# Kernel optimization log

Hardware: AMD Instinct MI355X
Metric: run time of the kernel (lower is better)

Reference implementation:

```python
import jax, jax.numpy as jnp
import numpy as np

T, B, H, E, V = 128, 64, 512, 256, 32000
UNK = 2
EPS = 1e-10


def setup_inputs() -> dict:
    key = jax.random.key(0)
    ks = jax.random.split(key, 16)
    s = 0.02
    return {
        "u_enc_out": jax.random.normal(ks[0], (T, B, H), jnp.float32),
        "z_tm1": jax.random.randint(ks[1], (1, B), 0, V),
        "last_hidden": jax.random.normal(ks[2], (1, B, H), jnp.float32),
        "u_input": jax.random.randint(ks[3], (T, B), 0, V),
        "emb": jax.random.normal(ks[4], (V, E), jnp.float32) * s,
        "attn_W": jax.random.normal(ks[5], (H, 2 * H), jnp.float32) * s,
        "attn_b": jnp.zeros((H,), jnp.float32),
        "attn_v": jax.random.normal(ks[6], (H,), jnp.float32) * (1.0 / np.sqrt(H)),
        "gru_Wih": jax.random.normal(ks[7], (3 * H, H + E), jnp.float32) * s,
        "gru_Whh": jax.random.normal(ks[8], (3 * H, H), jnp.float32) * s,
        "gru_bih": jnp.zeros((3 * H,), jnp.float32),
        "gru_bhh": jnp.zeros((3 * H,), jnp.float32),
        "proj_W": jax.random.normal(ks[9], (V, 2 * H), jnp.float32) * s,
        "proj_b": jnp.zeros((V,), jnp.float32),
        "copy1_W": jax.random.normal(ks[10], (H, H), jnp.float32) * s,
        "copy1_b": jnp.zeros((H,), jnp.float32),
    }


def _copy_logscore(raw, u_input):
    # raw: [B,T] copy scores; u_input: [T,B] int ids
    # Faithful to: log(bmm(exp(raw - max), sparse_one_hot_with_1e-10_floor)) + max
    cmax = jnp.max(raw, axis=1, keepdims=True)            # [B,1]
    ex = jnp.exp(raw - cmax)                              # [B,T]
    idx = u_input.T                                       # [B,T]
    idx = jnp.where(idx == UNK, V + jnp.arange(T)[None, :], idx)
    mask = (u_input.T != 0).astype(ex.dtype)
    total = jnp.sum(ex, axis=1)                           # [B] (all t, incl. ignored)
    scat = jax.vmap(lambda e, i: jnp.zeros((V + T,), ex.dtype).at[i].add(e))(ex * mask, idx)
    return jnp.log(EPS * total[:, None] + (1.0 - EPS) * scat) + cmax  # [B,V+T]


def reference(u_enc_out, z_tm1, last_hidden, u_input, emb, attn_W, attn_b, attn_v,
              gru_Wih, gru_Whh, gru_bih, gru_bhh, proj_W, proj_b, copy1_W, copy1_b):
    enc = jnp.transpose(u_enc_out, (1, 0, 2))             # [B,T,H]
    h = last_hidden[0]                                    # [B,H]
    # Attn: energy = tanh(Linear([h;enc])), score = v . energy, softmax over T
    Hrep = jnp.broadcast_to(h[:, None, :], enc.shape)
    energy = jnp.tanh(jnp.einsum('bti,hi->bth', jnp.concatenate([Hrep, enc], -1), attn_W) + attn_b)
    alpha = jax.nn.softmax(jnp.einsum('h,bth->bt', attn_v, energy), axis=1)
    ctx = jnp.einsum('bt,bth->bh', alpha, enc)            # [B,H]
    # GRU step (pytorch gate order r,z,n)
    x = jnp.concatenate([emb[z_tm1[0]], ctx], axis=-1)    # [B,E+H]
    gi = x @ gru_Wih.T + gru_bih
    gh = h @ gru_Whh.T + gru_bhh
    i_r, i_z, i_n = jnp.split(gi, 3, axis=-1)
    h_r, h_z, h_n = jnp.split(gh, 3, axis=-1)
    r = jax.nn.sigmoid(i_r + h_r)
    z = jax.nn.sigmoid(i_z + h_z)
    n = jnp.tanh(i_n + r * h_n)
    h_new = (1.0 - z) * n + z * h                         # [B,H]
    gru_out = h_new[None]                                 # [1,B,H]
    new_hidden = h_new[None]
    # generation score
    gen_score = jnp.concatenate([h_new, ctx], -1) @ proj_W.T + proj_b  # [B,V]
    # copy score
    cs = jnp.tanh(jnp.einsum('bth,ih->bti', enc, copy1_W) + copy1_b)   # [B,T,H]
    raw = jnp.einsum('bth,bh->bt', cs, h_new)             # [B,T]
    u_copy = _copy_logscore(raw, u_input)                 # [B,V+T]
    scores = jax.nn.softmax(jnp.concatenate([gen_score, u_copy], axis=1), axis=1)
    g, c = scores[:, :V], scores[:, V:]                   # [B,V], [B,V+T]
    proba = jnp.concatenate([g + c[:, :V], c[:, V:]], axis=1)  # [B,V+T]
    return gru_out, new_hidden, proba
```

## Files before the change

kernel.cpp:

```cpp
#include <hip/hip_runtime.h>
#include <math.h>

#define T_ 128
#define B_ 64
#define H_ 512
#define E_ 256
#define V_ 32000
#define VT_ (V_ + T_)
#define UNK_ 2
#define EPS_ 1e-10f
#define NP_ (V_ / 64)

typedef __attribute__((ext_vector_type(8))) _Float16 half8;
typedef __attribute__((ext_vector_type(2))) _Float16 half2v;
typedef __attribute__((ext_vector_type(4))) float floatx4;

#define NB_ZERO 32
#define NB_CVTA 512
#define NB_CVTC 512
#define NB_WH   8192
#define NB_CVTW 2048
#define NB_XE   64
#define NB_XH   128
#define NB_BC   8
#define NB_PRO (NB_ZERO + NB_CVTA + NB_CVTC + NB_WH + NB_CVTW + NB_XE + NB_XH + NB_BC)

__global__ __launch_bounds__(256) void prologue_k(
        const float* __restrict__ attn_W,
        const float* __restrict__ copy1_W, const float* __restrict__ last_h,
        const float* __restrict__ attn_b, const float* __restrict__ emb,
        const int* __restrict__ z, const float* __restrict__ Wih,
        const float* __restrict__ Whh, const float* __restrict__ bih,
        const float* __restrict__ bhh,
        float* __restrict__ zbase,
        _Float16* __restrict__ Wb_attn, _Float16* __restrict__ Wb_copy,
        float* __restrict__ Wh, _Float16* __restrict__ Wcat,
        _Float16* __restrict__ xg, float* __restrict__ bcat) {
    int bid = blockIdx.x, tid = threadIdx.x;
    if (bid < NB_ZERO) { zbase[bid * 256 + tid] = 0.f; return; }
    bid -= NB_ZERO;
    if (bid < NB_CVTA) {
        int c = tid * 2;
        float2 v = *(const float2*)(attn_W + (size_t)bid * 1024 + 512 + c);
        Wb_attn[bid * 512 + c]     = (_Float16)v.x;
        Wb_attn[bid * 512 + c + 1] = (_Float16)v.y;
        return;
    }
    bid -= NB_CVTA;
    if (bid < NB_CVTC) {
        int c = tid * 2;
        float2 v = *(const float2*)(copy1_W + (size_t)bid * 512 + c);
        Wb_copy[bid * 512 + c]     = (_Float16)v.x;
        Wb_copy[bid * 512 + c + 1] = (_Float16)v.y;
        return;
    }
    bid -= NB_CVTC;
    if (bid < NB_WH) {
        int wid = bid * 4 + (tid >> 6), lane = tid & 63;
        int b = wid >> 9, m = wid & 511;
        const float4* wr = (const float4*)(attn_W + (size_t)m * 1024);
        const float4* xr = (const float4*)(last_h + b * 512);
        float s = 0.f;
        #pragma unroll
        for (int i = 0; i < 2; ++i) {
            int k = lane + i * 64;
            float4 w = wr[k], x = xr[k];
            s += w.x * x.x + w.y * x.y + w.z * x.z + w.w * x.w;
        }
        #pragma unroll
        for (int off = 32; off > 0; off >>= 1) s += __shfl_down(s, off);
        if (lane == 0) Wh[b * 512 + m] = s + attn_b[m];
        return;
    }
    bid -= NB_WH;
    if (bid < NB_CVTW) {
        int mp = bid;
        int q  = (mp >> 4) & 3;
        int hh = (mp >> 6) * 16 + (mp & 15);
        #pragma unroll
        for (int j = 0; j < 5; ++j) {
            int c = j * 256 + tid;
            float w;
            if (q == 0)      w = (c < 768) ? Wih[(size_t)hh * 768 + c]
                                           : Whh[(size_t)hh * 512 + (c - 768)];
            else if (q == 1) w = (c < 768) ? Wih[(size_t)(512 + hh) * 768 + c]
                                           : Whh[(size_t)(512 + hh) * 512 + (c - 768)];
            else if (q == 2) w = (c < 768) ? Wih[(size_t)(1024 + hh) * 768 + c] : 0.f;
            else             w = (c >= 768) ? Whh[(size_t)(1024 + hh) * 512 + (c - 768)] : 0.f;
            Wcat[(size_t)mp * 1280 + c] = (_Float16)w;
        }
        return;
    }
    bid -= NB_CVTW;
    if (bid < NB_XE) {
        int idx = bid * 256 + tid;
        int bb = idx >> 8, c = idx & 255;
        xg[bb * 1280 + c] = (_Float16)emb[(size_t)z[bb] * E_ + c];
        return;
    }
    bid -= NB_XE;
    if (bid < NB_XH) {
        int idx = bid * 256 + tid;
        int bb = idx >> 9, c = idx & 511;
        xg[bb * 1280 + 768 + c] = (_Float16)last_h[bb * H_ + c];
        return;
    }
    bid -= NB_XH;
    {
        int mp = bid * 256 + tid;
        int q  = (mp >> 4) & 3;
        int hh = (mp >> 6) * 16 + (mp & 15);
        float v2;
        if (q == 0)      v2 = bih[hh] + bhh[hh];
        else if (q == 1) v2 = bih[512 + hh] + bhh[512 + hh];
        else if (q == 2) v2 = bih[1024 + hh];
        else             v2 = bhh[1024 + hh];
        bcat[mp] = v2;
    }
}

__global__ __launch_bounds__(512) void enc_dual_k(
        const float* __restrict__ u_enc,
        const _Float16* __restrict__ Wa,
        const _Float16* __restrict__ Wc,
        const float* __restrict__ Wh,
        const float* __restrict__ attn_v,
        const float* __restrict__ copy1_b,
        float* __restrict__ score,
        _Float16* __restrict__ cs) {
    __shared__ _Float16 As[64 * 512];
    int bid = blockIdx.x;
    int xcd = bid & 7, loc = bid >> 3;
    int xt = xcd * 16 + (loc & 15);
    int yt = loc >> 4;
    int b  = xt >> 1;
    int t0 = (xt & 1) * 64;
    int r0 = b * T_ + t0;
    int tid = threadIdx.x;
    int lane = tid & 63, wave = tid >> 6;
    const float* srcb = u_enc + (size_t)t0 * B_ * H_ + (size_t)b * H_;
    #pragma unroll
    for (int i = 0; i < 8; ++i) {
        int G = i * 512 + tid;
        int r = G >> 6, s = G & 63;
        const float4* p = (const float4*)(srcb + (size_t)r * B_ * H_ + s * 8);
        float4 a0 = p[0], a1 = p[1];
        half8 v;
        v[0] = (_Float16)a0.x; v[1] = (_Float16)a0.y; v[2] = (_Float16)a0.z; v[3] = (_Float16)a0.w;
        v[4] = (_Float16)a1.x; v[5] = (_Float16)a1.y; v[6] = (_Float16)a1.z; v[7] = (_Float16)a1.w;
        *(half8*)&As[(size_t)(((r << 6) | (s ^ (r & 7))) << 3)] = v;
    }
    __syncthreads();
    int n0 = yt * 128 + (wave >> 2) * 64 + (wave & 3) * 16;
    int coln = lane & 15;
    int g = lane >> 4;
    const _Float16* wra = Wa + (size_t)(n0 + coln) * H_ + g * 8;
    const _Float16* wrc = Wc + (size_t)(n0 + coln) * H_ + g * 8;
    floatx4 acca[4] = {}, accc[4] = {};
    #pragma unroll 4
    for (int k0 = 0; k0 < H_; k0 += 32) {
        half8 fba = *(const half8*)(wra + k0);
        half8 fbc = *(const half8*)(wrc + k0);
        #pragma unroll
        for (int mi = 0; mi < 4; ++mi) {
            int r = mi * 16 + coln;
            half8 fa = *(const half8*)&As[((size_t)r << 9) +
                          ((((k0 >> 3) + g) ^ (coln & 7)) << 3)];
            acca[mi] = __builtin_amdgcn_mfma_f32_16x16x32_f16(fa, fba, acca[mi], 0, 0, 0);
            accc[mi] = __builtin_amdgcn_mfma_f32_16x16x32_f16(fa, fbc, accc[mi], 0, 0, 0);
        }
    }
    int col = n0 + coln;
    float addt = Wh[b * H_ + col];
    float av   = attn_v[col];
    float cb   = copy1_b[col];
    int rbase = g * 4;
    #pragma unroll
    for (int mi = 0; mi < 4; ++mi)
        #pragma unroll
        for (int r = 0; r < 4; ++r) {
            int row = r0 + mi * 16 + rbase + r;
            float x = acca[mi][r] + addt;
            float t2 = __expf(2.f * x);
            float v = av * ((t2 - 1.f) / (t2 + 1.f));
            v += __shfl_xor(v, 1);
            v += __shfl_xor(v, 2);
            v += __shfl_xor(v, 4);
            v += __shfl_xor(v, 8);
            if (coln == 0) atomicAdd(&score[row], v);
            float y = accc[mi][r] + cb;
            float t3 = __expf(2.f * y);
            cs[(size_t)row * H_ + col] = (_Float16)((t3 - 1.f) / (t3 + 1.f));
        }
}

__global__ __launch_bounds__(128) void softctx_k(
        const float* __restrict__ score, const float* __restrict__ u_enc,
        _Float16* __restrict__ xcat, _Float16* __restrict__ xg) {
    __shared__ float al[T_];
    __shared__ float red[T_];
    int b = blockIdx.x, tid = threadIdx.x;
    float v = score[b * T_ + tid];
    red[tid] = v;
    __syncthreads();
    for (int s = 64; s > 0; s >>= 1) { if (tid < s) red[tid] = fmaxf(red[tid], red[tid + s]); __syncthreads(); }
    float m = red[0]; __syncthreads();
    float e = __expf(v - m);
    red[tid] = e;
    __syncthreads();
    for (int s = 64; s > 0; s >>= 1) { if (tid < s) red[tid] += red[tid + s]; __syncthreads(); }
    al[tid] = e / red[0];
    __syncthreads();
    int col0 = blockIdx.y * 256 + tid * 2;
    const float2* ebase = (const float2*)(u_enc + (size_t)b * H_ + col0);
    float s0 = 0.f, s1 = 0.f;
    #pragma unroll 16
    for (int t = 0; t < T_; ++t) {
        float2 u = ebase[(size_t)t * (B_ * H_ / 2)];
        float a = al[t];
        s0 += a * u.x;
        s1 += a * u.y;
    }
    half2v o; o[0] = (_Float16)s0; o[1] = (_Float16)s1;
    *(half2v*)(xcat + b * 1024 + 512 + col0) = o;
    *(half2v*)(xg + b * 1280 + 256 + col0)   = o;
}

__global__ __launch_bounds__(512) void grucat_k(
        const _Float16* __restrict__ xg,
        const _Float16* __restrict__ Wcat,
        const float* __restrict__ bcat,
        const float* __restrict__ hprev,
        float* __restrict__ out,
        _Float16* __restrict__ xcat) {
    __shared__ float Lt[8][64][17];
    int tid = threadIdx.x;
    int lane = tid & 63, wave = tid >> 6;
    int q = wave & 3, khalf = wave >> 2;
    int n0 = blockIdx.x * 64 + q * 16;
    int coln = lane & 15;
    int kq  = (lane >> 4) * 8;
    int kbase = khalf * 640;
    const _Float16* wrow  = Wcat + (size_t)(n0 + coln) * 1280 + kbase + kq;
    const _Float16* abase = xg + kbase + kq;
    floatx4 acc[4] = {};
    #pragma unroll 5
    for (int k0 = 0; k0 < 640; k0 += 32) {
        half8 fb = *(const half8*)(wrow + k0);
        #pragma unroll
        for (int mi = 0; mi < 4; ++mi) {
            half8 fa = *(const half8*)(abase + (size_t)(mi * 16 + coln) * 1280 + k0);
            acc[mi] = __builtin_amdgcn_mfma_f32_16x16x32_f16(fa, fb, acc[mi], 0, 0, 0);
        }
    }
    int rbase = (lane >> 4) * 4;
    #pragma unroll
    for (int mi = 0; mi < 4; ++mi)
        #pragma unroll
        for (int r = 0; r < 4; ++r)
            Lt[wave][mi * 16 + rbase + r][coln] = acc[mi][r];
    __syncthreads();
    int HB = blockIdx.x * 16;
    #pragma unroll
    for (int p = tid; p < 1024; p += 512) {
        int b = p >> 4, i = p & 15;
        float G0 = Lt[0][b][i] + Lt[4][b][i] + bcat[blockIdx.x * 64 + i];
        float G1 = Lt[1][b][i] + Lt[5][b][i] + bcat[blockIdx.x * 64 + 16 + i];
        float G2 = Lt[2][b][i] + Lt[6][b][i] + bcat[blockIdx.x * 64 + 32 + i];
        float G3 = Lt[3][b][i] + Lt[7][b][i] + bcat[blockIdx.x * 64 + 48 + i];
        float rr = 1.f / (1.f + __expf(-G0));
        float zz = 1.f / (1.f + __expf(-G1));
        float nn = tanhf(G2 + rr * G3);
        float h  = hprev[b * H_ + HB + i];
        float hv = (1.f - zz) * nn + zz * h;
        out[b * H_ + HB + i] = hv;
        out[B_ * H_ + b * H_ + HB + i] = hv;
        xcat[b * 1024 + HB + i] = (_Float16)hv;
    }
}

__global__ __launch_bounds__(256) void proj_stats_k(
        const _Float16* __restrict__ xcat,
        const float* __restrict__ Wp,
        const float* __restrict__ bp,
        float* __restrict__ gen,
        float* __restrict__ mpart, float* __restrict__ lpart) {
    __shared__ float m_lds[4][64];
    __shared__ float l_lds[4][64];
    int lane = threadIdx.x & 63;
    int wave = threadIdx.x >> 6;
    int n0 = (blockIdx.x * 4 + wave) * 16;
    int coln = lane & 15;
    int kq  = (lane >> 4) * 8;
    const float* wrow = Wp + (size_t)(n0 + coln) * 1024 + kq;
    const _Float16* abase = xcat + kq;
    floatx4 acc[4] = {};
    #pragma unroll 8
    for (int k0 = 0; k0 < 1024; k0 += 32) {
        const float4* wb = (const float4*)(wrow + k0);
        float4 w0 = wb[0], w1 = wb[1];
        half8 fb;
        fb[0] = (_Float16)w0.x; fb[1] = (_Float16)w0.y; fb[2] = (_Float16)w0.z; fb[3] = (_Float16)w0.w;
        fb[4] = (_Float16)w1.x; fb[5] = (_Float16)w1.y; fb[6] = (_Float16)w1.z; fb[7] = (_Float16)w1.w;
        #pragma unroll
        for (int mi = 0; mi < 4; ++mi) {
            half8 fa = *(const half8*)(abase + (size_t)(mi * 16 + coln) * 1024 + k0);
            acc[mi] = __builtin_amdgcn_mfma_f32_16x16x32_f16(fa, fb, acc[mi], 0, 0, 0);
        }
    }
    int rbase = (lane >> 4) * 4;
    float bias = bp[n0 + coln];
    #pragma unroll
    for (int mi = 0; mi < 4; ++mi)
        #pragma unroll
        for (int r = 0; r < 4; ++r) {
            int brow = mi * 16 + rbase + r;
            float x = acc[mi][r] + bias;
            gen[(size_t)brow * V_ + n0 + coln] = x;
            float mm = x;
            mm = fmaxf(mm, __shfl_xor(mm, 1));
            mm = fmaxf(mm, __shfl_xor(mm, 2));
            mm = fmaxf(mm, __shfl_xor(mm, 4));
            mm = fmaxf(mm, __shfl_xor(mm, 8));
            float e = __expf(x - mm);
            e += __shfl_xor(e, 1);
            e += __shfl_xor(e, 2);
            e += __shfl_xor(e, 4);
            e += __shfl_xor(e, 8);
            if (coln == 0) { m_lds[wave][brow] = mm; l_lds[wave][brow] = e; }
        }
    __syncthreads();
    if (threadIdx.x < 64) {
        int bb = threadIdx.x;
        float M = m_lds[0][bb], L = l_lds[0][bb];
        #pragma unroll
        for (int w = 1; w < 4; ++w) {
            float m2 = m_lds[w][bb], l2 = l_lds[w][bb];
            float nm = fmaxf(M, m2);
            L = L * __expf(M - nm) + l2 * __expf(m2 - nm);
            M = nm;
        }
        mpart[bb * NP_ + blockIdx.x] = M;
        lpart[bb * NP_ + blockIdx.x] = L;
    }
}

__global__ __launch_bounds__(512) void raw_epi_k(
        const _Float16* __restrict__ cs, const float* __restrict__ hnew,
        const int* __restrict__ u_input,
        const float* __restrict__ mpart, const float* __restrict__ lpart,
        float* __restrict__ scat, float* __restrict__ params) {
    __shared__ float rawS[T_];
    __shared__ float red[T_];
    __shared__ float ms[512], ls[512];
    int b = blockIdx.x, tid = threadIdx.x;
    int lane = tid & 63, wave = tid >> 6;
    const float4* hp = (const float4*)(hnew + b * H_ + lane * 8);
    float4 ha = hp[0], hb = hp[1];
    #pragma unroll 4
    for (int i = 0; i < 16; ++i) {
        int t = wave * 16 + i;
        half8 c8 = *(const half8*)(cs + (size_t)(b * T_ + t) * H_ + lane * 8);
        float s = (float)c8[0] * ha.x + (float)c8[1] * ha.y + (float)c8[2] * ha.z + (float)c8[3] * ha.w
                + (float)c8[4] * hb.x + (float)c8[5] * hb.y + (float)c8[6] * hb.z + (float)c8[7] * hb.w;
        #pragma unroll
        for (int off = 32; off > 0; off >>= 1) s += __shfl_down(s, off);
        if (lane == 0) rawS[t] = s;
    }
    __syncthreads();
    int t = tid;
    float v = (t < T_) ? rawS[t] : -1e30f;
    if (t < T_) red[t] = v;
    __syncthreads();
    for (int s = 64; s > 0; s >>= 1) { if (t < s) red[t] = fmaxf(red[t], red[t + s]); __syncthreads(); }
    float cm = red[0]; __syncthreads();
    float e = (t < T_) ? __expf(v - cm) : 0.f;
    if (t < T_) red[t] = e;
    __syncthreads();
    for (int s = 64; s > 0; s >>= 1) { if (t < s) red[t] += red[t + s]; __syncthreads(); }
    float tot = red[0]; __syncthreads();
    int id = (t < T_) ? u_input[t * B_ + b] : 0;
    size_t j = (size_t)b * VT_ + ((id == UNK_) ? (V_ + t) : id);
    if (id != 0) scat[j] = 0.f;
    __syncthreads();
    if (id != 0) atomicAdd(&scat[j], e);
    if (t < T_) red[t] = (id != 0) ? e : 0.f;
    __syncthreads();
    for (int s = 64; s > 0; s >>= 1) { if (t < s) red[t] += red[t + s]; __syncthreads(); }
    float ssum = red[0]; __syncthreads();
    float sv = (id != 0) ? scat[j] : 0.f;
    if (t < T_) red[t] = sv;
    __syncthreads();
    for (int s = 64; s > 0; s >>= 1) { if (t < s) red[t] = fmaxf(red[t], red[t + s]); __syncthreads(); }
    float smax = red[0]; __syncthreads();
    float M = -1e30f, L = 0.f;
    if (t < NP_) { M = mpart[b * NP_ + t]; L = lpart[b * NP_ + t]; }
    ms[t] = M; ls[t] = L;
    __syncthreads();
    for (int s = 256; s > 0; s >>= 1) {
        if (t < s) {
            float m2 = ms[t + s], l2 = ls[t + s];
            float nm = fmaxf(ms[t], m2);
            ls[t] = ls[t] * __expf(ms[t] - nm) + l2 * __expf(m2 - nm);
            ms[t] = nm;
        }
        __syncthreads();
    }
    if (t == 0) {
        float Mg = ms[0], Zg = ls[0];
        float umax = cm + logf(EPS_ * tot + (1.f - EPS_) * smax);
        float M2 = fmaxf(Mg, umax);
        float coef = __expf(cm - M2);
        float Z = Zg * __expf(Mg - M2) + coef * (EPS_ * tot * (float)VT_ + (1.f - EPS_) * ssum);
        float invZ = 1.f / Z;
        params[b * 4 + 0] = M2;
        params[b * 4 + 1] = invZ;
        params[b * 4 + 2] = coef * EPS_ * tot * invZ;
        params[b * 4 + 3] = coef * (1.f - EPS_) * invZ;
    }
}

__global__ __launch_bounds__(256) void write_k(const float* __restrict__ gen,
                                               const float* __restrict__ params,
                                               float* __restrict__ proba) {
    int b = blockIdx.y;
    int i4 = blockIdx.x * 256 + threadIdx.x;
    if (i4 >= VT_ / 4) return;
    float M = params[b * 4], invZ = params[b * 4 + 1], addc = params[b * 4 + 2];
    int j = i4 * 4;
    float4 p;
    if (j < V_) {
        float4 g = *(const float4*)(gen + (size_t)b * V_ + j);
        p.x = addc + __expf(g.x - M) * invZ;
        p.y = addc + __expf(g.y - M) * invZ;
        p.z = addc + __expf(g.z - M) * invZ;
        p.w = addc + __expf(g.w - M) * invZ;
    } else {
        p.x = p.y = p.z = p.w = addc;
    }
    *(float4*)(proba + (size_t)b * VT_ + j) = p;
}

__global__ void fix_k(const float* __restrict__ gen, const float* __restrict__ scat,
                      const int* __restrict__ u_input, const float* __restrict__ params,
                      float* __restrict__ proba) {
    int b = blockIdx.x, t = threadIdx.x;
    int id = u_input[t * B_ + b];
    if (id == 0) return;
    int j = (id == UNK_) ? (V_ + t) : id;
    float M = params[b * 4], invZ = params[b * 4 + 1];
    float addc = params[b * 4 + 2], scoef = params[b * 4 + 3];
    float p = addc + scoef * scat[(size_t)b * VT_ + j];
    if (j < V_) p += __expf(gen[(size_t)b * V_ + j] - M) * invZ;
    proba[(size_t)b * VT_ + j] = p;
}

extern "C" void kernel_launch(void* const* d_in, const int* in_sizes, int n_in,
                              void* d_out, int out_size, void* d_ws, size_t ws_size,
                              hipStream_t stream) {
    const float* u_enc   = (const float*)d_in[0];
    const int*   z_tm1   = (const int*)d_in[1];
    const float* last_h  = (const float*)d_in[2];
    const int*   u_input = (const int*)d_in[3];
    const float* emb     = (const float*)d_in[4];
    const float* attn_W  = (const float*)d_in[5];
    const float* attn_b  = (const float*)d_in[6];
    const float* attn_v  = (const float*)d_in[7];
    const float* gru_Wih = (const float*)d_in[8];
    const float* gru_Whh = (const float*)d_in[9];
    const float* gru_bih = (const float*)d_in[10];
    const float* gru_bhh = (const float*)d_in[11];
    const float* proj_W  = (const float*)d_in[12];
    const float* proj_b  = (const float*)d_in[13];
    const float* copy1_W = (const float*)d_in[14];
    const float* copy1_b = (const float*)d_in[15];
    float* out = (float*)d_out;

    float* ws    = (float*)d_ws;
    float* score = ws;
    float* gen   = score + B_ * T_;
    float* scat  = gen + (size_t)B_ * V_;
    float* Wh    = scat + (size_t)B_ * VT_;
    float* mpart = Wh + B_ * H_;
    float* lpart = mpart + B_ * NP_;
    float* params= lpart + B_ * NP_;
    float* bcat  = params + B_ * 4;
    _Float16* xcat  = (_Float16*)(bcat + 2048);
    _Float16* xg    = xcat + B_ * 1024;
    _Float16* Wb_attn = xg + B_ * 1280;
    _Float16* Wb_copy = Wb_attn + H_ * H_;
    _Float16* Wcat  = Wb_copy + H_ * H_;
    _Float16* cs    = Wcat + 2048 * 1280;

    prologue_k<<<NB_PRO, 256, 0, stream>>>(attn_W, copy1_W, last_h, attn_b,
                                           emb, z_tm1, gru_Wih, gru_Whh, gru_bih, gru_bhh,
                                           score, Wb_attn, Wb_copy, Wh, Wcat, xg, bcat);

    enc_dual_k<<<512, 512, 0, stream>>>(u_enc, Wb_attn, Wb_copy, Wh, attn_v, copy1_b,
                                        score, cs);

    softctx_k<<<dim3(B_, 2), 128, 0, stream>>>(score, u_enc, xcat, xg);

    grucat_k<<<32, 512, 0, stream>>>(xg, Wcat, bcat, last_h, out, xcat);

    proj_stats_k<<<NP_, 256, 0, stream>>>(xcat, proj_W, proj_b, gen, mpart, lpart);

    raw_epi_k<<<B_, 512, 0, stream>>>(cs, out, u_input, mpart, lpart, scat, params);

    float* proba = out + 2 * B_ * H_;
    write_k<<<dim3((VT_ / 4 + 255) / 256, B_), 256, 0, stream>>>(gen, params, proba);
    fix_k<<<B_, T_, 0, stream>>>(gen, scat, u_input, params, proba);
}
```

Baseline: 355.5 us.

## Fuse copy-score epilogue into projection launch and merge write with fix

The copy-score raw/scatter blocks now run as extra blocks of the projection GEMM launch, so the two run concurrently instead of back to back. The final softmax normalisation is folded into a combined write+fix kernel. Each block of that kernel redundantly reduces the 500 partial max/sum pairs for its row, then writes probabilities and patches copied positions inside its own 1024-element range. This removes two kernel launches and their serialization. The cost is redundant per-block reductions and heterogeneous blocks within one grid.

Measured after the change: 353.5 us. Within noise of the previous version (-0.6%).

```diff
diff --git a/kernel.cpp b/kernel.cpp
--- a/kernel.cpp
+++ b/kernel.cpp
@@ -279,87 +279,87 @@
     }
 }
 
-__global__ __launch_bounds__(256) void proj_stats_k(
+__global__ __launch_bounds__(256) void proj_raw_k(
         const _Float16* __restrict__ xcat,
         const float* __restrict__ Wp,
         const float* __restrict__ bp,
         float* __restrict__ gen,
-        float* __restrict__ mpart, float* __restrict__ lpart) {
+        float* __restrict__ mpart, float* __restrict__ lpart,
+        const _Float16* __restrict__ cs,
+        const float* __restrict__ hnew,
+        const int* __restrict__ u_input,
+        float* __restrict__ scat, float* __restrict__ sc4) {
     __shared__ float m_lds[4][64];
     __shared__ float l_lds[4][64];
-    int lane = threadIdx.x & 63;
-    int wave = threadIdx.x >> 6;
-    int n0 = (blockIdx.x * 4 + wave) * 16;
-    int coln = lane & 15;
-    int kq  = (lane >> 4) * 8;
-    const float* wrow = Wp + (size_t)(n0 + coln) * 1024 + kq;
-    const _Float16* abase = xcat + kq;
-    floatx4 acc[4] = {};
-    #pragma unroll 8
-    for (int k0 = 0; k0 < 1024; k0 += 32) {
-        const float4* wb = (const float4*)(wrow + k0);
-        float4 w0 = wb[0], w1 = wb[1];
-        half8 fb;
-        fb[0] = (_Float16)w0.x; fb[1] = (_Float16)w0.y; fb[2] = (_Float16)w0.z; fb[3] = (_Float16)w0.w;
-        fb[4] = (_Float16)w1.x; fb[5] = (_Float16)w1.y; fb[6] = (_Float16)w1.z; fb[7] = (_Float16)w1.w;
-        #pragma unroll
-        for (int mi = 0; mi < 4; ++mi) {
-            half8 fa = *(const half8*)(abase + (size_t)(mi * 16 + coln) * 1024 + k0);
-            acc[mi] = __builtin_amdgcn_mfma_f32_16x16x32_f16(fa, fb, acc[mi], 0, 0, 0);
-        }
-    }
-    int rbase = (lane >> 4) * 4;
-    float bias = bp[n0 + coln];
-    #pragma unroll
-    for (int mi = 0; mi < 4; ++mi)
-        #pragma unroll
-        for (int r = 0; r < 4; ++r) {
-            int brow = mi * 16 + rbase + r;
-            float x = acc[mi][r] + bias;
-            gen[(size_t)brow * V_ + n0 + coln] = x;
-            float mm = x;
-            mm = fmaxf(mm, __shfl_xor(mm, 1));
-            mm = fmaxf(mm, __shfl_xor(mm, 2));
-            mm = fmaxf(mm, __shfl_xor(mm, 4));
-            mm = fmaxf(mm, __shfl_xor(mm, 8));
-            float e = __expf(x - mm);
-            e += __shfl_xor(e, 1);
-            e += __shfl_xor(e, 2);
-            e += __shfl_xor(e, 4);
-            e += __shfl_xor(e, 8);
-            if (coln == 0) { m_lds[wave][brow] = mm; l_lds[wave][brow] = e; }
-        }
-    __syncthreads();
-    if (threadIdx.x < 64) {
-        int bb = threadIdx.x;
-        float M = m_lds[0][bb], L = l_lds[0][bb];
-        #pragma unroll
-        for (int w = 1; w < 4; ++w) {
-            float m2 = m_lds[w][bb], l2 = l_lds[w][bb];
-            float nm = fmaxf(M, m2);
-            L = L * __expf(M - nm) + l2 * __expf(m2 - nm);
-            M = nm;
-        }
-        mpart[bb * NP_ + blockIdx.x] = M;
-        lpart[bb * NP_ + blockIdx.x] = L;
-    }
-}
-
-__global__ __launch_bounds__(512) void raw_epi_k(
-        const _Float16* __restrict__ cs, const float* __restrict__ hnew,
-        const int* __restrict__ u_input,
-        const float* __restrict__ mpart, const float* __restrict__ lpart,
-        float* __restrict__ scat, float* __restrict__ params) {
     __shared__ float rawS[T_];
     __shared__ float red[T_];
-    __shared__ float ms[512], ls[512];
-    int b = blockIdx.x, tid = threadIdx.x;
+    if (blockIdx.x < NP_) {
+        int lane = threadIdx.x & 63;
+        int wave = threadIdx.x >> 6;
+        int n0 = (blockIdx.x * 4 + wave) * 16;
+        int coln = lane & 15;
+        int kq  = (lane >> 4) * 8;
+        const float* wrow = Wp + (size_t)(n0 + coln) * 1024 + kq;
+        const _Float16* abase = xcat + kq;
+        floatx4 acc[4] = {};
+        #pragma unroll 8
+        for (int k0 = 0; k0 < 1024; k0 += 32) {
+            const float4* wb = (const float4*)(wrow + k0);
+            float4 w0 = wb[0], w1 = wb[1];
+            half8 fb;
+            fb[0] = (_Float16)w0.x; fb[1] = (_Float16)w0.y; fb[2] = (_Float16)w0.z; fb[3] = (_Float16)w0.w;
+            fb[4] = (_Float16)w1.x; fb[5] = (_Float16)w1.y; fb[6] = (_Float16)w1.z; fb[7] = (_Float16)w1.w;
+            #pragma unroll
+            for (int mi = 0; mi < 4; ++mi) {
+                half8 fa = *(const half8*)(abase + (size_t)(mi * 16 + coln) * 1024 + k0);
+                acc[mi] = __builtin_amdgcn_mfma_f32_16x16x32_f16(fa, fb, acc[mi], 0, 0, 0);
+            }
+        }
+        int rbase = (lane >> 4) * 4;
+        float bias = bp[n0 + coln];
+        #pragma unroll
+        for (int mi = 0; mi < 4; ++mi)
+            #pragma unroll
+            for (int r = 0; r < 4; ++r) {
+                int brow = mi * 16 + rbase + r;
+                float x = acc[mi][r] + bias;
+                gen[(size_t)brow * V_ + n0 + coln] = x;
+                float mm = x;
+                mm = fmaxf(mm, __shfl_xor(mm, 1));
+                mm = fmaxf(mm, __shfl_xor(mm, 2));
+                mm = fmaxf(mm, __shfl_xor(mm, 4));
+                mm = fmaxf(mm, __shfl_xor(mm, 8));
+                float e = __expf(x - mm);
+                e += __shfl_xor(e, 1);
+                e += __shfl_xor(e, 2);
+                e += __shfl_xor(e, 4);
+                e += __shfl_xor(e, 8);
+                if (coln == 0) { m_lds[wave][brow] = mm; l_lds[wave][brow] = e; }
+            }
+        __syncthreads();
+        if (threadIdx.x < 64) {
+            int bb = threadIdx.x;
+            float M = m_lds[0][bb], L = l_lds[0][bb];
+            #pragma unroll
+            for (int w = 1; w < 4; ++w) {
+                float m2 = m_lds[w][bb], l2 = l_lds[w][bb];
+                float nm = fmaxf(M, m2);
+                L = L * __expf(M - nm) + l2 * __expf(m2 - nm);
+                M = nm;
+            }
+            mpart[bb * NP_ + blockIdx.x] = M;
+            lpart[bb * NP_ + blockIdx.x] = L;
+        }
+        return;
+    }
+    int b = blockIdx.x - NP_;
+    int tid = threadIdx.x;
     int lane = tid & 63, wave = tid >> 6;
     const float4* hp = (const float4*)(hnew + b * H_ + lane * 8);
     float4 ha = hp[0], hb = hp[1];
     #pragma unroll 4
-    for (int i = 0; i < 16; ++i) {
-        int t = wave * 16 + i;
+    for (int i = 0; i < 32; ++i) {
+        int t = wave * 32 + i;
         half8 c8 = *(const half8*)(cs + (size_t)(b * T_ + t) * H_ + lane * 8);
         float s = (float)c8[0] * ha.x + (float)c8[1] * ha.y + (float)c8[2] * ha.z + (float)c8[3] * ha.w
                 + (float)c8[4] * hb.x + (float)c8[5] * hb.y + (float)c8[6] * hb.z + (float)c8[7] * hb.w;
@@ -392,67 +392,84 @@
     if (t < T_) red[t] = sv;
     __syncthreads();
     for (int s = 64; s > 0; s >>= 1) { if (t < s) red[t] = fmaxf(red[t], red[t + s]); __syncthreads(); }
-    float smax = red[0]; __syncthreads();
+    if (t == 0) {
+        sc4[b * 4 + 0] = cm;
+        sc4[b * 4 + 1] = tot;
+        sc4[b * 4 + 2] = ssum;
+        sc4[b * 4 + 3] = red[0];
+    }
+}
+
+__global__ __launch_bounds__(256) void write_fix_k(
+        const float* __restrict__ gen,
+        const float* __restrict__ mpart, const float* __restrict__ lpart,
+        const float* __restrict__ sc4, const int* __restrict__ u_input,
+        const float* __restrict__ scat, float* __restrict__ proba) {
+    __shared__ float ms[256], ls[256];
+    __shared__ float pb[4];
+    int b = blockIdx.y, tid = threadIdx.x;
     float M = -1e30f, L = 0.f;
-    if (t < NP_) { M = mpart[b * NP_ + t]; L = lpart[b * NP_ + t]; }
-    ms[t] = M; ls[t] = L;
-    __syncthreads();
-    for (int s = 256; s > 0; s >>= 1) {
-        if (t < s) {
-            float m2 = ms[t + s], l2 = ls[t + s];
-            float nm = fmaxf(ms[t], m2);
-            ls[t] = ls[t] * __expf(ms[t] - nm) + l2 * __expf(m2 - nm);
-            ms[t] = nm;
+    for (int s = tid; s < NP_; s += 256) {
+        float m2 = mpart[b * NP_ + s], l2 = lpart[b * NP_ + s];
+        float nm = fmaxf(M, m2);
+        L = L * __expf(M - nm) + l2 * __expf(m2 - nm);
+        M = nm;
+    }
+    ms[tid] = M; ls[tid] = L;
+    __syncthreads();
+    for (int s = 128; s > 0; s >>= 1) {
+        if (tid < s) {
+            float m2 = ms[tid + s], l2 = ls[tid + s];
+            float nm = fmaxf(ms[tid], m2);
+            ls[tid] = ls[tid] * __expf(ms[tid] - nm) + l2 * __expf(m2 - nm);
+            ms[tid] = nm;
         }
         __syncthreads();
     }
-    if (t == 0) {
+    if (tid == 0) {
         float Mg = ms[0], Zg = ls[0];
+        float cm = sc4[b * 4], tot = sc4[b * 4 + 1], ssum = sc4[b * 4 + 2], smax = sc4[b * 4 + 3];
         float umax = cm + logf(EPS_ * tot + (1.f - EPS_) * smax);
         float M2 = fmaxf(Mg, umax);
         float coef = __expf(cm - M2);
         float Z = Zg * __expf(Mg - M2) + coef * (EPS_ * tot * (float)VT_ + (1.f - EPS_) * ssum);
         float invZ = 1.f / Z;
-        params[b * 4 + 0] = M2;
-        params[b * 4 + 1] = invZ;
-        params[b * 4 + 2] = coef * EPS_ * tot * invZ;
-        params[b * 4 + 3] = coef * (1.f - EPS_) * invZ;
-    }
-}
-
-__global__ __launch_bounds__(256) void write_k(const float* __restrict__ gen,
-                                               const float* __restrict__ params,
-                                               float* __restrict__ proba) {
-    int b = blockIdx.y;
-    int i4 = blockIdx.x * 256 + threadIdx.x;
-    if (i4 >= VT_ / 4) return;
-    float M = params[b * 4], invZ = params[b * 4 + 1], addc = params[b * 4 + 2];
-    int j = i4 * 4;
-    float4 p;
-    if (j < V_) {
-        float4 g = *(const float4*)(gen + (size_t)b * V_ + j);
-        p.x = addc + __expf(g.x - M) * invZ;
-        p.y = addc + __expf(g.y - M) * invZ;
-        p.z = addc + __expf(g.z - M) * invZ;
-        p.w = addc + __expf(g.w - M) * invZ;
-    } else {
-        p.x = p.y = p.z = p.w = addc;
-    }
-    *(float4*)(proba + (size_t)b * VT_ + j) = p;
-}
-
-__global__ void fix_k(const float* __restrict__ gen, const float* __restrict__ scat,
-                      const int* __restrict__ u_input, const float* __restrict__ params,
-                      float* __restrict__ proba) {
-    int b = blockIdx.x, t = threadIdx.x;
-    int id = u_input[t * B_ + b];
-    if (id == 0) return;
-    int j = (id == UNK_) ? (V_ + t) : id;
-    float M = params[b * 4], invZ = params[b * 4 + 1];
-    float addc = params[b * 4 + 2], scoef = params[b * 4 + 3];
-    float p = addc + scoef * scat[(size_t)b * VT_ + j];
-    if (j < V_) p += __expf(gen[(size_t)b * V_ + j] - M) * invZ;
-    proba[(size_t)b * VT_ + j] = p;
+        pb[0] = M2;
+        pb[1] = invZ;
+        pb[2] = coef * EPS_ * tot * invZ;
+        pb[3] = coef * (1.f - EPS_) * invZ;
+    }
+    __syncthreads();
+    float M2 = pb[0], invZ = pb[1], addc = pb[2], scoef = pb[3];
+    int i4 = blockIdx.x * 256 + tid;
+    if (i4 < VT_ / 4) {
+        int j = i4 * 4;
+        float4 p;
+        if (j < V_) {
+            float4 g = *(const float4*)(gen + (size_t)b * V_ + j);
+            p.x = addc + __expf(g.x - M2) * invZ;
+            p.y = addc + __expf(g.y - M2) * invZ;
+            p.z = addc + __expf(g.z - M2) * invZ;
+            p.w = addc + __expf(g.w - M2) * invZ;
+        } else {
+            p.x = p.y = p.z = p.w = addc;
+        }
+        *(float4*)(proba + (size_t)b * VT_ + j) = p;
+    }
+    __syncthreads();
+    if (tid < T_) {
+        int t = tid;
+        int id = u_input[t * B_ + b];
+        if (id != 0) {
+            int j = (id == UNK_) ? (V_ + t) : id;
+            int lo = blockIdx.x * 1024;
+            if (j >= lo && j < lo + 1024) {
+                float p = addc + scoef * scat[(size_t)b * VT_ + j];
+                if (j < V_) p += __expf(gen[(size_t)b * V_ + j] - M2) * invZ;
+                proba[(size_t)b * VT_ + j] = p;
+            }
+        }
+    }
 }
 
 extern "C" void kernel_launch(void* const* d_in, const int* in_sizes, int n_in,
@@ -483,8 +500,8 @@
     float* Wh    = scat + (size_t)B_ * VT_;
     float* mpart = Wh + B_ * H_;
     float* lpart = mpart + B_ * NP_;
-    float* params= lpart + B_ * NP_;
-    float* bcat  = params + B_ * 4;
+    float* sc4   = lpart + B_ * NP_;
+    float* bcat  = sc4 + B_ * 4;
     _Float16* xcat  = (_Float16*)(bcat + 2048);
     _Float16* xg    = xcat + B_ * 1024;
     _Float16* Wb_attn = xg + B_ * 1280;
@@ -503,11 +520,10 @@
 
     grucat_k<<<32, 512, 0, stream>>>(xg, Wcat, bcat, last_h, out, xcat);
 
-    proj_stats_k<<<NP_, 256, 0, stream>>>(xcat, proj_W, proj_b, gen, mpart, lpart);
-
-    raw_epi_k<<<B_, 512, 0, stream>>>(cs, out, u_input, mpart, lpart, scat, params);
+    proj_raw_k<<<NP_ + B_, 256, 0, stream>>>(xcat, proj_W, proj_b, gen, mpart, lpart,
+                                             cs, out, u_input, scat, sc4);
 
     float* proba = out + 2 * B_ * H_;
-    write_k<<<dim3((VT_ / 4 + 255) / 256, B_), 256, 0, stream>>>(gen, params, proba);
-    fix_k<<<B_, T_, 0, stream>>>(gen, scat, u_input, params, proba);
-}
+    write_fix_k<<<dim3((VT_ / 4 + 255) / 256, B_), 256, 0, stream>>>(
+        gen, mpart, lpart, sc4, u_input, scat, proba);
+}
```
